# Performance work log

Measured on AMD Instinct MI355X. Metric: run time of the kernel, lower is better.

## Reference

```python
import jax, jax.numpy as jnp
import numpy as np
from jax import lax

B, N, W, F = 16, 2000, 32, 5
TH, SH, HEADS = 128, 64, 4
C = SH // HEADS          # per-head out channels = 16
E_BASE = 32000           # base edges per graph


def setup_inputs():
    key = jax.random.key(0)
    ks = jax.random.split(key, 24)
    rn = lambda k, s, sc=0.05: (jax.random.normal(k, s, jnp.float32) * sc)
    inp = {
        'x': jax.random.normal(ks[0], (B, N, W, F), jnp.float32),
        'base_edge_index': jax.random.randint(ks[1], (2, E_BASE), 0, N, jnp.int64),
        # GRU layer 0 (input F -> TH), layer 1 (TH -> TH); PyTorch gate order r,z,n
        'W_ih0': rn(ks[2], (3 * TH, F)), 'W_hh0': rn(ks[3], (3 * TH, TH)),
        'b_ih0': rn(ks[4], (3 * TH,)),   'b_hh0': rn(ks[5], (3 * TH,)),
        'W_ih1': rn(ks[6], (3 * TH, TH)), 'W_hh1': rn(ks[7], (3 * TH, TH)),
        'b_ih1': rn(ks[8], (3 * TH,)),   'b_hh1': rn(ks[9], (3 * TH,)),
        'ln1_g': jnp.ones((TH,), jnp.float32), 'ln1_b': jnp.zeros((TH,), jnp.float32),
        # GATConv: lin (no bias), att_src/att_dst [H,C], output bias [H*C]
        'gat_W': rn(ks[10], (TH, HEADS * C)),
        'att_src': rn(ks[11], (HEADS, C)), 'att_dst': rn(ks[12], (HEADS, C)),
        'gat_b': rn(ks[13], (HEADS * C,)),
        'ln2_g': jnp.ones((SH,), jnp.float32), 'ln2_b': jnp.zeros((SH,), jnp.float32),
        'reg_W1': rn(ks[14], (SH, 32)), 'reg_b1': rn(ks[15], (32,)),
        'reg_W2': rn(ks[16], (32, 1)),  'reg_b2': rn(ks[17], (1,)),
    }
    return inp


def _gru_layer(xs, W_ih, W_hh, b_ih, b_hh):
    # xs: [W, M, Din] time-major; returns (h_T [M,TH], ys [W,M,TH])
    M = xs.shape[1]
    h0 = jnp.zeros((M, W_hh.shape[1]), xs.dtype)

    def step(h, x_t):
        gi = x_t @ W_ih.T + b_ih
        gh = h @ W_hh.T + b_hh
        i_r, i_z, i_n = jnp.split(gi, 3, axis=-1)
        h_r, h_z, h_n = jnp.split(gh, 3, axis=-1)
        r = jax.nn.sigmoid(i_r + h_r)
        z = jax.nn.sigmoid(i_z + h_z)
        n = jnp.tanh(i_n + r * h_n)
        h_new = (1.0 - z) * n + z * h
        return h_new, h_new

    return lax.scan(step, h0, xs)


def _layernorm(x, g, b, eps=1e-5):
    mu = jnp.mean(x, -1, keepdims=True)
    var = jnp.var(x, -1, keepdims=True)
    return (x - mu) * lax.rsqrt(var + eps) * g + b


def _forward(x, base_edge_index, W_ih0, W_hh0, b_ih0, b_hh0, W_ih1, W_hh1,
             b_ih1, b_hh1, ln1_g, ln1_b, gat_W, att_src, att_dst, gat_b,
             ln2_g, ln2_b, reg_W1, reg_b1, reg_W2, reg_b2):
    Bv, Nv, Wv, Fv = x.shape
    M = Bv * Nv
    xs = x.reshape(M, Wv, Fv).transpose(1, 0, 2)  # [W, M, F] time-major
    _, ys0 = _gru_layer(xs, W_ih0, W_hh0, b_ih0, b_hh0)
    h1, _ = _gru_layer(ys0, W_ih1, W_hh1, b_ih1, b_hh1)  # hidden[-1]: [M, TH]
    temb = _layernorm(h1, ln1_g, ln1_b)

    # batched edge index with per-graph node offsets + self loops (PyG default)
    offs = (jnp.arange(Bv, dtype=base_edge_index.dtype) * Nv)
    eb = (base_edge_index[:, None, :] + offs[None, :, None]).reshape(2, -1)
    loops = jnp.arange(M, dtype=base_edge_index.dtype)
    src = jnp.concatenate([eb[0], loops])
    dst = jnp.concatenate([eb[1], loops])

    # GATConv
    xp = (temb @ gat_W).reshape(M, HEADS, C)                 # [M,H,C]
    a_src = jnp.sum(xp * att_src, -1)                        # [M,H]
    a_dst = jnp.sum(xp * att_dst, -1)
    alpha = jax.nn.leaky_relu(a_src[src] + a_dst[dst], 0.2)  # [E,H]
    amax = jax.ops.segment_max(alpha, dst, num_segments=M)
    ex = jnp.exp(alpha - amax[dst])
    den = jax.ops.segment_sum(ex, dst, num_segments=M)
    w = ex / den[dst]                                        # segment softmax
    agg = jax.ops.segment_sum(w[:, :, None] * xp[src], dst, num_segments=M)
    semb = agg.reshape(M, HEADS * C) + gat_b

    semb = jax.nn.leaky_relu(_layernorm(semb, ln2_g, ln2_b), 0.2)
    h = jax.nn.leaky_relu(semb @ reg_W1 + reg_b1, 0.2)
    pred = h @ reg_W2 + reg_b2                               # [M,1]
    return pred.reshape(Bv, Nv)


def reference(x, base_edge_index, W_ih0, W_hh0, b_ih0, b_hh0, W_ih1, W_hh1,
              b_ih1, b_hh1, ln1_g, ln1_b, gat_W, att_src, att_dst, gat_b,
              ln2_g, ln2_b, reg_W1, reg_b1, reg_W2, reg_b2):
    return _forward(x, base_edge_index, W_ih0, W_hh0, b_ih0, b_hh0, W_ih1,
                    W_hh1, b_ih1, b_hh1, ln1_g, ln1_b, gat_W, att_src,
                    att_dst, gat_b, ln2_g, ln2_b, reg_W1, reg_b1, reg_W2,
                    reg_b2)
```

## Files before the change

kernel.cpp:

```cpp
#include <hip/hip_runtime.h>
#include <math.h>

#define B_   16
#define N_   2000
#define W_   32
#define F_   5
#define TH_  128
#define M_   (B_*N_)
#define SH_  64
#define NPB  128

typedef unsigned short u16;
typedef short short8 __attribute__((ext_vector_type(8)));
typedef float f32x4  __attribute__((ext_vector_type(4)));

__device__ __forceinline__ float leaky_(float x) { return x > 0.0f ? x : 0.2f * x; }
__device__ __forceinline__ float sigm_(float x) {
  return __fdividef(1.0f, 1.0f + __expf(-x));
}
__device__ __forceinline__ float tanh_(float x) {
  const float e2 = __expf(2.0f * x);
  return 1.0f - __fdividef(2.0f, e2 + 1.0f);
}

__device__ __forceinline__ u16 f2bf(float f) {
  unsigned u = __float_as_uint(f);
  unsigned r = (u + 0x7FFFu + ((u >> 16) & 1u)) >> 16;
  return (u16)r;
}
__device__ __forceinline__ u16 f2bf_tr(float f) {
  return (u16)(__float_as_uint(f) >> 16);
}
__device__ __forceinline__ float bf2f(u16 h) { return __uint_as_float(((unsigned)h) << 16); }

__device__ __forceinline__ f32x4 mfma3(short8 ah, short8 al, short8 bh, short8 bl, f32x4 c) {
  c = __builtin_amdgcn_mfma_f32_16x16x32_bf16(ah, bh, c, 0, 0, 0);
  c = __builtin_amdgcn_mfma_f32_16x16x32_bf16(al, bh, c, 0, 0, 0);
  c = __builtin_amdgcn_mfma_f32_16x16x32_bf16(ah, bl, c, 0, 0, 0);
  return c;
}

#define S0_ (384*32)
#define S1_ (384*128)
#define XS_ (M_*W_*8)

__global__ void splitA_kernel(const float* __restrict__ Wih0,
                              u16* __restrict__ wih0h, u16* __restrict__ wih0l)
{
  const int i = blockIdx.x * 256 + threadIdx.x;
  if (i >= S0_) return;
  const int row = i >> 5, k = i & 31;
  const float v = (k < F_) ? Wih0[row * F_ + k] : 0.0f;
  const int g = row >> 7, unit = row & 127, wv = unit >> 4, li = unit & 15;
  const int qq = k >> 3, j = k & 7;
  const int p = ((wv * 3 + g) * 64 + qq * 16 + li) * 8 + j;
  const u16 h = f2bf(v);
  wih0h[p] = h;
  wih0l[p] = f2bf(v - bf2f(h));
}

__global__ __launch_bounds__(256)
void splitB_kernel(const float* __restrict__ Whh0, const float* __restrict__ Wih1,
                   const float* __restrict__ Whh1,
                   u16* __restrict__ wpk, u16* __restrict__ wlo)
{
  const int w = blockIdx.x * 4 + (threadIdx.x >> 6);
  const int lane = threadIdx.x & 63;
  const int mat = w / 384;
  const int r = w - mat * 384;
  const float* src = (mat == 0) ? Whh0 : (mat == 1) ? Wih1 : Whh1;
  const int g = r >> 7, unit = r & 127, wv = unit >> 4, li = unit & 15;

#pragma unroll
  for (int e = 0; e < 2; ++e) {
    const int k = lane * 2 + e;
    const float v = src[r * TH_ + k];
    const u16 h = f2bf(v);
    const u16 l = f2bf(v - bf2f(h));
    const int kt = k >> 5, rem = k & 31, qq = rem >> 3, j = rem & 7;
    const int p = (((wv * 3 + mat) * 4 + kt) * 3 + g) * 512 + (qq * 16 + li) * 8 + j;
    wpk[p] = h;
    wlo[p] = l;
  }
}

__global__ __launch_bounds__(256)
void splitX_kernel(const float* __restrict__ x,
                   u16* __restrict__ xh, u16* __restrict__ xl)
{
  const int tid = blockIdx.x * 256 + threadIdx.x;
  if (tid >= M_ * W_) return;
  const int li = tid & 15, nt = (tid >> 4) & 7, t = (tid >> 7) & 31, mb = tid >> 12;
  const int m = mb * 128 + nt * 16 + li;
  const float* px = x + (size_t)m * (W_ * F_) + t * F_;
  short8 vh, vl;
#pragma unroll
  for (int j = 0; j < 8; ++j) {
    const float v = (j < F_) ? px[j] : 0.0f;
    const u16 h = f2bf_tr(v);
    vh[j] = (short)h;
    vl[j] = (short)f2bf(v - bf2f(h));
  }
  *(short8*)(xh + (size_t)tid * 8) = vh;
  *(short8*)(xl + (size_t)tid * 8) = vl;
}

__global__ __launch_bounds__(512, 2)
void gru_mfma_kernel(const u16* __restrict__ xpkh, const u16* __restrict__ xpkl,
                     const u16* __restrict__ wih0h, const u16* __restrict__ wih0l,
                     const u16* __restrict__ wpk, const u16* __restrict__ wlo,
                     const float* __restrict__ bih0, const float* __restrict__ bhh0,
                     const float* __restrict__ bih1, const float* __restrict__ bhh1,
                     const float* __restrict__ ln1g, const float* __restrict__ ln1b,
                     float* __restrict__ temb)
{
  __shared__ u16 h0hi[NPB * TH_], h0lo[NPB * TH_];
  __shared__ u16 h1hi[NPB * TH_], h1lo[NPB * TH_];

  const int tid = threadIdx.x;
  const int lane = tid & 63, wv = tid >> 6, q = lane >> 4, li = lane & 15;
  const int mbase = blockIdx.x * NPB;
  const int unit = wv * 16 + li;
  const int laneo = lane * 8;
  const int wbase = wv * 18432;

  for (int i = tid; i < NPB * TH_ / 2; i += 512) {
    ((unsigned*)h0hi)[i] = 0u; ((unsigned*)h0lo)[i] = 0u;
    ((unsigned*)h1hi)[i] = 0u; ((unsigned*)h1lo)[i] = 0u;
  }

  const float BR0  = bih0[unit] + bhh0[unit];
  const float BZ0  = bih0[TH_ + unit] + bhh0[TH_ + unit];
  const float BNI0 = bih0[2 * TH_ + unit];
  const float BNH0 = bhh0[2 * TH_ + unit];
  const float BR1  = bih1[unit] + bhh1[unit];
  const float BZ1  = bih1[TH_ + unit] + bhh1[TH_ + unit];
  const float BNI1 = bih1[2 * TH_ + unit];
  const float BNH1 = bhh1[2 * TH_ + unit];
  const f32x4 z4 = {0.0f, 0.0f, 0.0f, 0.0f};
  const short8 z8 = {0, 0, 0, 0, 0, 0, 0, 0};

  short8 bih0h_[3], bih0l_[3];
#pragma unroll
  for (int g = 0; g < 3; ++g) {
    const int ro = (wv * 3 + g) * 512 + laneo;
    bih0h_[g] = *(const short8*)(wih0h + ro);
    bih0l_[g] = *(const short8*)(wih0l + ro);
  }

  int nbase[4];
#pragma unroll
  for (int r = 0; r < 4; ++r)
    nbase[r] = (q * 4 + r) * TH_ + ((((unit >> 3) ^ (q * 4 + r))) << 3) + (unit & 7);

  __syncthreads();

  f32x4 aR[8], aZ[8], aNI[8], aNH[8];

  for (int t = 0; t < W_; ++t) {
    {
      const u16* xbh = xpkh + ((size_t)(blockIdx.x * W_ + t) * 8) * 128 + li * 8;
      const u16* xbl = xpkl + ((size_t)(blockIdx.x * W_ + t) * 8) * 128 + li * 8;
#pragma unroll
      for (int nt = 0; nt < 8; ++nt) {
        short8 xh8 = z8, xl8 = z8;
        if (q == 0) {
          xh8 = *(const short8*)(xbh + nt * 128);
          xl8 = *(const short8*)(xbl + nt * 128);
        }
#pragma unroll
        for (int g = 0; g < 3; ++g) {
          const f32x4 c = mfma3(xh8, xl8, bih0h_[g], bih0l_[g], z4);
          if (g == 0) aR[nt] = c; else if (g == 1) aZ[nt] = c; else aNI[nt] = c;
        }
      }
    }

#pragma unroll
    for (int kt = 0; kt < 4; ++kt) {
      const int off = wbase + kt * 1536 + laneo;
      const short8 bh0 = *(const short8*)(wpk + off);
      const short8 bl0 = *(const short8*)(wlo + off);
      const short8 bh1 = *(const short8*)(wpk + off + 512);
      const short8 bl1 = *(const short8*)(wlo + off + 512);
      const short8 bh2 = *(const short8*)(wpk + off + 1024);
      const short8 bl2 = *(const short8*)(wlo + off + 1024);
      const int ko = ((kt * 4 + q) ^ li) * 8;
#pragma unroll
      for (int nt = 0; nt < 8; ++nt) {
        const int ab = (nt * 16 + li) * TH_ + ko;
        const short8 Ah = *(const short8*)(h0hi + ab);
        const short8 Al = *(const short8*)(h0lo + ab);
        aR[nt] = mfma3(Ah, Al, bh0, bl0, aR[nt]);
        aZ[nt] = mfma3(Ah, Al, bh1, bl1, aZ[nt]);
        aNH[nt] = mfma3(Ah, Al, bh2, bl2, (kt == 0) ? z4 : aNH[nt]);
      }
    }
    __syncthreads();

#pragma unroll
    for (int nt = 0; nt < 8; ++nt)
#pragma unroll
      for (int r = 0; r < 4; ++r) {
        const int idx = nt * 2048 + nbase[r];
        const float hold = bf2f(h0hi[idx]) + bf2f(h0lo[idx]);
        const float rr = sigm_(aR[nt][r] + BR0);
        const float zz = sigm_(aZ[nt][r] + BZ0);
        const float nn = tanh_(aNI[nt][r] + BNI0 + rr * (aNH[nt][r] + BNH0));
        const float hv = (1.0f - zz) * nn + zz * hold;
        const u16 hh = f2bf_tr(hv);
        h0hi[idx] = hh;
        h0lo[idx] = f2bf(hv - bf2f(hh));
      }
    __syncthreads();

#pragma unroll
    for (int kt = 0; kt < 4; ++kt) {
      const int off = wbase + 6144 + kt * 1536 + laneo;
      const short8 bh0 = *(const short8*)(wpk + off);
      const short8 bl0 = *(const short8*)(wlo + off);
      const short8 bh1 = *(const short8*)(wpk + off + 512);
      const short8 bl1 = *(const short8*)(wlo + off + 512);
      const short8 bh2 = *(const short8*)(wpk + off + 1024);
      const short8 bl2 = *(const short8*)(wlo + off + 1024);
      const int ko = ((kt * 4 + q) ^ li) * 8;
#pragma unroll
      for (int nt = 0; nt < 8; ++nt) {
        const int ab = (nt * 16 + li) * TH_ + ko;
        const short8 Ah = *(const short8*)(h0hi + ab);
        const short8 Al = *(const short8*)(h0lo + ab);
        aR[nt]  = mfma3(Ah, Al, bh0, bl0, (kt == 0) ? z4 : aR[nt]);
        aZ[nt]  = mfma3(Ah, Al, bh1, bl1, (kt == 0) ? z4 : aZ[nt]);
        aNI[nt] = mfma3(Ah, Al, bh2, bl2, (kt == 0) ? z4 : aNI[nt]);
      }
    }
#pragma unroll
    for (int kt = 0; kt < 4; ++kt) {
      const int off = wbase + 12288 + kt * 1536 + laneo;
      const short8 bh0 = *(const short8*)(wpk + off);
      const short8 bl0 = *(const short8*)(wlo + off);
      const short8 bh1 = *(const short8*)(wpk + off + 512);
      const short8 bl1 = *(const short8*)(wlo + off + 512);
      const short8 bh2 = *(const short8*)(wpk + off + 1024);
      const short8 bl2 = *(const short8*)(wlo + off + 1024);
      const int ko = ((kt * 4 + q) ^ li) * 8;
#pragma unroll
      for (int nt = 0; nt < 8; ++nt) {
        const int ab = (nt * 16 + li) * TH_ + ko;
        const short8 Ah = *(const short8*)(h1hi + ab);
        const short8 Al = *(const short8*)(h1lo + ab);
        aR[nt]  = mfma3(Ah, Al, bh0, bl0, aR[nt]);
        aZ[nt]  = mfma3(Ah, Al, bh1, bl1, aZ[nt]);
        aNH[nt] = mfma3(Ah, Al, bh2, bl2, (kt == 0) ? z4 : aNH[nt]);
      }
    }
    __syncthreads();

#pragma unroll
    for (int nt = 0; nt < 8; ++nt)
#pragma unroll
      for (int r = 0; r < 4; ++r) {
        const int idx = nt * 2048 + nbase[r];
        const float hold = bf2f(h1hi[idx]) + bf2f(h1lo[idx]);
        const float rr = sigm_(aR[nt][r] + BR1);
        const float zz = sigm_(aZ[nt][r] + BZ1);
        const float nn = tanh_(aNI[nt][r] + BNI1 + rr * (aNH[nt][r] + BNH1));
        const float hv = (1.0f - zz) * nn + zz * hold;
        const u16 hh = f2bf_tr(hv);
        h1hi[idx] = hh;
        h1lo[idx] = f2bf(hv - bf2f(hh));
      }
    __syncthreads();
  }

  const int n = tid >> 2, qq = tid & 3;
  float vr[32];
  float s = 0.0f;
#pragma unroll
  for (int g8 = 0; g8 < 4; ++g8) {
    const int k0 = qq * 32 + g8 * 8;
    const int g16 = (((k0 >> 3) ^ (n & 15))) * 8;
    const short8 hv = *(const short8*)(h1hi + n * TH_ + g16);
    const short8 lv = *(const short8*)(h1lo + n * TH_ + g16);
#pragma unroll
    for (int j = 0; j < 8; ++j) {
      const float f = bf2f((u16)hv[j]) + bf2f((u16)lv[j]);
      vr[g8 * 8 + j] = f;
      s += f;
    }
  }
  s += __shfl_xor(s, 1, 64); s += __shfl_xor(s, 2, 64);
  const float mu = s * (1.0f / TH_);
  float s2 = 0.0f;
#pragma unroll
  for (int k = 0; k < 32; ++k) { const float d = vr[k] - mu; s2 += d * d; }
  s2 += __shfl_xor(s2, 1, 64); s2 += __shfl_xor(s2, 2, 64);
  const float inv = rsqrtf(s2 * (1.0f / TH_) + 1e-5f);
  float* to = temb + (size_t)(mbase + n) * TH_ + qq * 32;
#pragma unroll
  for (int k = 0; k < 32; ++k)
    to[k] = (vr[k] - mu) * inv * ln1g[qq * 32 + k] + ln1b[qq * 32 + k];
}

__global__ __launch_bounds__(256)
void gat_xp_kernel(const float* __restrict__ temb, const float* __restrict__ gatW,
                   const float* __restrict__ attS, const float* __restrict__ attD,
                   float* __restrict__ xp, float* __restrict__ asrc, float* __restrict__ adst)
{
  __shared__ float ts[64][TH_ + 4];
  __shared__ float4 ws4[TH_][16];
  __shared__ float sa[64], sd[64];

  const int tid = threadIdx.x;
  const int mbase = blockIdx.x * 64;

  for (int i = tid; i < 64 * TH_; i += 256) {
    const int n = i >> 7, k = i & 127;
    ts[n][k] = temb[(size_t)mbase * TH_ + i];
  }
  for (int i = tid; i < TH_ * 16; i += 256)
    ((float4*)ws4)[i] = ((const float4*)gatW)[i];
  if (tid < 64) { sa[tid] = attS[tid]; sd[tid] = attD[tid]; }
  __syncthreads();

  const int nl = tid >> 2;
  const int q  = tid & 3;
  float4 acc[4];
#pragma unroll
  for (int i = 0; i < 4; ++i) acc[i] = make_float4(0.f, 0.f, 0.f, 0.f);

  for (int k = 0; k < TH_; ++k) {
    const float tv = ts[nl][k];
#pragma unroll
    for (int c0 = 0; c0 < 4; ++c0) {
      const float4 wv = ws4[k][q * 4 + c0];
      acc[c0].x += tv * wv.x; acc[c0].y += tv * wv.y;
      acc[c0].z += tv * wv.z; acc[c0].w += tv * wv.w;
    }
  }

  float as = 0.0f, ad = 0.0f;
#pragma unroll
  for (int c0 = 0; c0 < 4; ++c0) {
    const int base = q * 16 + c0 * 4;
    as += acc[c0].x * sa[base + 0] + acc[c0].y * sa[base + 1] +
          acc[c0].z * sa[base + 2] + acc[c0].w * sa[base + 3];
    ad += acc[c0].x * sd[base + 0] + acc[c0].y * sd[base + 1] +
          acc[c0].z * sd[base + 2] + acc[c0].w * sd[base + 3];
  }

  const int m = mbase + nl;
  asrc[m * 4 + q] = as;
  adst[m * 4 + q] = ad;
  float4* xpo = (float4*)&xp[(size_t)m * 64 + q * 16];
#pragma unroll
  for (int c0 = 0; c0 < 4; ++c0) xpo[c0] = acc[c0];
}

__global__ void hist_kernel(const int* __restrict__ ei, const int EB, int* __restrict__ cnt)
{
  const int e = blockIdx.x * 256 + threadIdx.x;
  if (e < EB) atomicAdd(&cnt[ei[EB + e]], 1);
}

__global__ void scan_kernel(const int* __restrict__ cnt, int* __restrict__ offs,
                            int* __restrict__ cursor)
{
  __shared__ int part[256];
  const int tid = threadIdx.x;
  const int c0 = tid * 8;
  int loc[8];
  int s = 0;
#pragma unroll
  for (int j = 0; j < 8; ++j) {
    const int idx = c0 + j;
    const int v = (idx < N_) ? cnt[idx] : 0;
    loc[j] = s; s += v;
  }
  part[tid] = s;
  __syncthreads();
  for (int o = 1; o < 256; o <<= 1) {
    const int v = (tid >= o) ? part[tid - o] : 0;
    __syncthreads();
    part[tid] += v;
    __syncthreads();
  }
  const int base = (tid > 0) ? part[tid - 1] : 0;
#pragma unroll
  for (int j = 0; j < 8; ++j) {
    const int idx = c0 + j;
    if (idx < N_) { offs[idx] = base + loc[j]; cursor[idx] = base + loc[j]; }
  }
  if (tid == 255) offs[N_] = part[255];
}

__global__ void fill_kernel(const int* __restrict__ ei, const int EB,
                            int* __restrict__ cursor, int* __restrict__ ssrc)
{
  const int e = blockIdx.x * 256 + threadIdx.x;
  if (e < EB) {
    const int d = ei[EB + e];
    const int p = atomicAdd(&cursor[d], 1);
    ssrc[p] = ei[e];
  }
}

__global__ __launch_bounds__(256)
void gather_kernel(const int* __restrict__ offs, const int* __restrict__ ssrc,
                   const float* __restrict__ asrc, const float* __restrict__ adst,
                   const float* __restrict__ xp,
                   const float* __restrict__ gatb,
                   const float* __restrict__ ln2g, const float* __restrict__ ln2b,
                   const float* __restrict__ W1, const float* __restrict__ b1,
                   const float* __restrict__ W2, const float* __restrict__ b2,
                   float* __restrict__ out)
{
  __shared__ float sW1[SH_ * 32];
  __shared__ float sb1[32], sW2[32];
  __shared__ float ssemb[4][SH_ + 1];

  const int tid = threadIdx.x;
  for (int i = tid; i < SH_ * 32; i += 256) sW1[i] = W1[i];
  if (tid < 32) { sb1[tid] = b1[tid]; sW2[tid] = W2[tid]; }
  __syncthreads();

  const int lane = tid & 63, grp = tid >> 6;
  const int m = blockIdx.x * 4 + grp;
  const int b = m / N_;
  const int n = m - b * N_;
  const int h = lane >> 4;

  const float adv = adst[m * 4 + h];
  const int o0 = offs[n], o1 = offs[n + 1];
  float accn = 0.0f, accd = 0.0f;
  for (int j = o0; j < o1; ++j) {
    const int s = ssrc[j] + b * N_;
    const float a = asrc[s * 4 + h];
    const float ex = __expf(leaky_(a + adv));
    accn += ex * xp[(size_t)s * 64 + lane];
    accd += ex;
  }
  {
    const float a = asrc[m * 4 + h];
    const float ex = __expf(leaky_(a + adv));
    accn += ex * xp[(size_t)m * 64 + lane];
    accd += ex;
  }

  const float v = accn / accd + gatb[lane];
  float s1 = v;
#pragma unroll
  for (int o = 32; o >= 1; o >>= 1) s1 += __shfl_xor(s1, o, 64);
  const float mu = s1 * (1.0f / 64.0f);
  const float d0 = v - mu;
  float s2 = d0 * d0;
#pragma unroll
  for (int o = 32; o >= 1; o >>= 1) s2 += __shfl_xor(s2, o, 64);
  const float var = s2 * (1.0f / 64.0f);
  float sem = d0 * rsqrtf(var + 1e-5f) * ln2g[lane] + ln2b[lane];
  sem = leaky_(sem);

  ssemb[grp][lane] = sem;
  __syncthreads();

  float contrib = 0.0f;
  if (lane < 32) {
    float acc = sb1[lane];
    for (int c = 0; c < SH_; ++c) acc += ssemb[grp][c] * sW1[c * 32 + lane];
    acc = leaky_(acc);
    contrib = acc * sW2[lane];
  }
#pragma unroll
  for (int o = 32; o >= 1; o >>= 1) contrib += __shfl_xor(contrib, o, 64);
  if (lane == 0) out[m] = contrib + b2[0];
}

extern "C" void kernel_launch(void* const* d_in, const int* in_sizes, int n_in,
                              void* d_out, int out_size, void* d_ws, size_t ws_size,
                              hipStream_t stream)
{
  const float* x    = (const float*)d_in[0];
  const int*   ei   = (const int*)d_in[1];
  const float* Wih0 = (const float*)d_in[2];
  const float* Whh0 = (const float*)d_in[3];
  const float* bih0 = (const float*)d_in[4];
  const float* bhh0 = (const float*)d_in[5];
  const float* Wih1 = (const float*)d_in[6];
  const float* Whh1 = (const float*)d_in[7];
  const float* bih1 = (const float*)d_in[8];
  const float* bhh1 = (const float*)d_in[9];
  const float* ln1g = (const float*)d_in[10];
  const float* ln1b = (const float*)d_in[11];
  const float* gatW = (const float*)d_in[12];
  const float* attS = (const float*)d_in[13];
  const float* attD = (const float*)d_in[14];
  const float* gatb = (const float*)d_in[15];
  const float* ln2g = (const float*)d_in[16];
  const float* ln2b = (const float*)d_in[17];
  const float* W1   = (const float*)d_in[18];
  const float* b1   = (const float*)d_in[19];
  const float* W2   = (const float*)d_in[20];
  const float* b2   = (const float*)d_in[21];
  float* out = (float*)d_out;

  const int EB = in_sizes[1] / 2;

  float* ws = (float*)d_ws;
  float* temb = ws;
  float* xp   = temb + (size_t)M_ * TH_;
  float* asrc = xp + (size_t)M_ * 64;
  float* adst = asrc + (size_t)M_ * 4;
  u16*   wh   = (u16*)(adst + (size_t)M_ * 4);
  u16* wih0h = wh;
  u16* wih0l = wh + S0_;
  u16* wpk   = wh + 2 * S0_;
  u16* wlo   = wpk + 3 * S1_;
  u16* xpkh  = wlo + 3 * S1_;
  u16* xpkl  = xpkh + XS_;
  int* cnt    = (int*)(xpkl + XS_);
  int* offs   = cnt + N_;
  int* cursor = offs + N_ + 1;
  int* ssrc   = cursor + N_;

  splitA_kernel<<<(S0_ + 255) / 256, 256, 0, stream>>>(Wih0, wih0h, wih0l);
  splitB_kernel<<<(3 * 384) / 4, 256, 0, stream>>>(Whh0, Wih1, Whh1, wpk, wlo);
  splitX_kernel<<<(M_ * W_) / 256, 256, 0, stream>>>(x, xpkh, xpkl);

  hipMemsetAsync(cnt, 0, N_ * sizeof(int), stream);
  hist_kernel<<<(EB + 255) / 256, 256, 0, stream>>>(ei, EB, cnt);
  scan_kernel<<<1, 256, 0, stream>>>(cnt, offs, cursor);
  fill_kernel<<<(EB + 255) / 256, 256, 0, stream>>>(ei, EB, cursor, ssrc);

  gru_mfma_kernel<<<M_ / NPB, 512, 0, stream>>>(
      xpkh, xpkl, wih0h, wih0l, wpk, wlo,
      bih0, bhh0, bih1, bhh1, ln1g, ln1b, temb);

  gat_xp_kernel<<<M_ / 64, 256, 0, stream>>>(temb, gatW, attS, attD, xp, asrc, adst);

  gather_kernel<<<M_ / 4, 256, 0, stream>>>(offs, ssrc, asrc, adst, xp,
                                            gatb, ln2g, ln2b, W1, b1, W2, b2, out);
}
```

Baseline: 1.483 ms.

## Quantize low-bf16 weight residuals to int8 and software-pipeline weight loads in GRU

The low part of each split-bf16 recurrent weight is now stored as int8 with a per-row scale and decoded in registers, which halves the global/L2 traffic for the residual weights. Weight fragments are double-buffered so the next k-tile's loads are issued before the current tile's MFMAs run. The full __syncthreads barriers are replaced with an LDS-only waitcnt plus s_barrier. The residual loses some precision, and the decode adds ALU work and register pressure.

```diff
diff --git a/kernel.cpp b/kernel.cpp
--- a/kernel.cpp
+++ b/kernel.cpp
@@ -38,6 +38,24 @@
   c = __builtin_amdgcn_mfma_f32_16x16x32_bf16(al, bh, c, 0, 0, 0);
   c = __builtin_amdgcn_mfma_f32_16x16x32_bf16(ah, bl, c, 0, 0, 0);
   return c;
+}
+
+__device__ __forceinline__ short8 dec8(int2 p, float s) {
+  short8 r;
+#pragma unroll
+  for (int j = 0; j < 4; ++j) {
+    const int e0 = (int)(signed char)((p.x >> (8 * j)) & 0xFF);
+    const int e1 = (int)(signed char)((p.y >> (8 * j)) & 0xFF);
+    r[j]     = (short)(__float_as_uint((float)e0 * s) >> 16);
+    r[4 + j] = (short)(__float_as_uint((float)e1 * s) >> 16);
+  }
+  return r;
+}
+
+__device__ __forceinline__ void bar_lds() {
+  asm volatile("s_waitcnt lgkmcnt(0)" ::: "memory");
+  __builtin_amdgcn_s_barrier();
+  asm volatile("" ::: "memory");
 }
 
 #define S0_ (384*32)
@@ -62,7 +80,8 @@
 __global__ __launch_bounds__(256)
 void splitB_kernel(const float* __restrict__ Whh0, const float* __restrict__ Wih1,
                    const float* __restrict__ Whh1,
-                   u16* __restrict__ wpk, u16* __restrict__ wlo)
+                   u16* __restrict__ wpk, signed char* __restrict__ wq,
+                   float* __restrict__ sInv)
 {
   const int w = blockIdx.x * 4 + (threadIdx.x >> 6);
   const int lane = threadIdx.x & 63;
@@ -71,17 +90,29 @@
   const float* src = (mat == 0) ? Whh0 : (mat == 1) ? Wih1 : Whh1;
   const int g = r >> 7, unit = r & 127, wv = unit >> 4, li = unit & 15;
 
-#pragma unroll
-  for (int e = 0; e < 2; ++e) {
-    const int k = lane * 2 + e;
-    const float v = src[r * TH_ + k];
-    const u16 h = f2bf(v);
-    const u16 l = f2bf(v - bf2f(h));
-    const int kt = k >> 5, rem = k & 31, qq = rem >> 3, j = rem & 7;
+  const float v0 = src[r * TH_ + lane * 2];
+  const float v1 = src[r * TH_ + lane * 2 + 1];
+  const u16 h0 = f2bf(v0), h1 = f2bf(v1);
+  const float l0 = v0 - bf2f(h0), l1 = v1 - bf2f(h1);
+  float m = fmaxf(fabsf(l0), fabsf(l1));
+#pragma unroll
+  for (int o = 32; o >= 1; o >>= 1) m = fmaxf(m, __shfl_xor(m, o, 64));
+  const float s = (m > 0.0f) ? __fdividef(127.0f, m) : 0.0f;
+  int q0 = (int)rintf(l0 * s), q1 = (int)rintf(l1 * s);
+  q0 = max(-127, min(127, q0)); q1 = max(-127, min(127, q1));
+
+  const int k0 = lane * 2, k1 = lane * 2 + 1;
+  {
+    const int kt = k0 >> 5, rem = k0 & 31, qq = rem >> 3, j = rem & 7;
     const int p = (((wv * 3 + mat) * 4 + kt) * 3 + g) * 512 + (qq * 16 + li) * 8 + j;
-    wpk[p] = h;
-    wlo[p] = l;
-  }
+    wpk[p] = h0; wq[p] = (signed char)q0;
+  }
+  {
+    const int kt = k1 >> 5, rem = k1 & 31, qq = rem >> 3, j = rem & 7;
+    const int p = (((wv * 3 + mat) * 4 + kt) * 3 + g) * 512 + (qq * 16 + li) * 8 + j;
+    wpk[p] = h1; wq[p] = (signed char)q1;
+  }
+  if (lane == 0) sInv[mat * 384 + r] = (m > 0.0f) ? m * (1.0f / 127.0f) : 0.0f;
 }
 
 __global__ __launch_bounds__(256)
@@ -91,7 +122,7 @@
   const int tid = blockIdx.x * 256 + threadIdx.x;
   if (tid >= M_ * W_) return;
   const int li = tid & 15, nt = (tid >> 4) & 7, t = (tid >> 7) & 31, mb = tid >> 12;
-  const int m = mb * 128 + nt * 16 + li;
+  const int m = mb * NPB + nt * 16 + li;
   const float* px = x + (size_t)m * (W_ * F_) + t * F_;
   short8 vh, vl;
 #pragma unroll
@@ -105,10 +136,20 @@
   *(short8*)(xl + (size_t)tid * 8) = vl;
 }
 
+#define WPREF(PN)                                                       \
+  { const int o_ = wbase + (PN) * 1536 + laneo;                         \
+    wbh[(PN) & 1][0] = *(const short8*)(wpk + o_);                      \
+    wbh[(PN) & 1][1] = *(const short8*)(wpk + o_ + 512);                \
+    wbh[(PN) & 1][2] = *(const short8*)(wpk + o_ + 1024);               \
+    wbq[(PN) & 1][0] = *(const int2*)(wqk + o_);                        \
+    wbq[(PN) & 1][1] = *(const int2*)(wqk + o_ + 512);                  \
+    wbq[(PN) & 1][2] = *(const int2*)(wqk + o_ + 1024); }
+
 __global__ __launch_bounds__(512, 2)
 void gru_mfma_kernel(const u16* __restrict__ xpkh, const u16* __restrict__ xpkl,
                      const u16* __restrict__ wih0h, const u16* __restrict__ wih0l,
-                     const u16* __restrict__ wpk, const u16* __restrict__ wlo,
+                     const u16* __restrict__ wpk, const signed char* __restrict__ wqk,
+                     const float* __restrict__ sInv,
                      const float* __restrict__ bih0, const float* __restrict__ bhh0,
                      const float* __restrict__ bih1, const float* __restrict__ bhh1,
                      const float* __restrict__ ln1g, const float* __restrict__ ln1b,
@@ -129,6 +170,13 @@
     ((unsigned*)h1hi)[i] = 0u; ((unsigned*)h1lo)[i] = 0u;
   }
 
+  float si0[3], si1[3], si2[3];
+#pragma unroll
+  for (int g = 0; g < 3; ++g) {
+    si0[g] = sInv[0 * 384 + g * TH_ + unit];
+    si1[g] = sInv[1 * 384 + g * TH_ + unit];
+    si2[g] = sInv[2 * 384 + g * TH_ + unit];
+  }
   const float BR0  = bih0[unit] + bhh0[unit];
   const float BZ0  = bih0[TH_ + unit] + bhh0[TH_ + unit];
   const float BNI0 = bih0[2 * TH_ + unit];
@@ -153,7 +201,11 @@
   for (int r = 0; r < 4; ++r)
     nbase[r] = (q * 4 + r) * TH_ + ((((unit >> 3) ^ (q * 4 + r))) << 3) + (unit & 7);
 
-  __syncthreads();
+  short8 wbh[2][3];
+  int2   wbq[2][3];
+  WPREF(0);
+
+  bar_lds();
 
   f32x4 aR[8], aZ[8], aNI[8], aNH[8];
 
@@ -178,25 +230,23 @@
 
 #pragma unroll
     for (int kt = 0; kt < 4; ++kt) {
-      const int off = wbase + kt * 1536 + laneo;
-      const short8 bh0 = *(const short8*)(wpk + off);
-      const short8 bl0 = *(const short8*)(wlo + off);
-      const short8 bh1 = *(const short8*)(wpk + off + 512);
-      const short8 bl1 = *(const short8*)(wlo + off + 512);
-      const short8 bh2 = *(const short8*)(wpk + off + 1024);
-      const short8 bl2 = *(const short8*)(wlo + off + 1024);
+      WPREF(kt + 1);
+      const short8 bh0 = wbh[kt & 1][0], bh1 = wbh[kt & 1][1], bh2 = wbh[kt & 1][2];
+      const short8 bl0 = dec8(wbq[kt & 1][0], si0[0]);
+      const short8 bl1 = dec8(wbq[kt & 1][1], si0[1]);
+      const short8 bl2 = dec8(wbq[kt & 1][2], si0[2]);
       const int ko = ((kt * 4 + q) ^ li) * 8;
 #pragma unroll
       for (int nt = 0; nt < 8; ++nt) {
         const int ab = (nt * 16 + li) * TH_ + ko;
         const short8 Ah = *(const short8*)(h0hi + ab);
         const short8 Al = *(const short8*)(h0lo + ab);
-        aR[nt] = mfma3(Ah, Al, bh0, bl0, aR[nt]);
-        aZ[nt] = mfma3(Ah, Al, bh1, bl1, aZ[nt]);
+        aR[nt]  = mfma3(Ah, Al, bh0, bl0, aR[nt]);
+        aZ[nt]  = mfma3(Ah, Al, bh1, bl1, aZ[nt]);
         aNH[nt] = mfma3(Ah, Al, bh2, bl2, (kt == 0) ? z4 : aNH[nt]);
       }
     }
-    __syncthreads();
+    bar_lds();
 
 #pragma unroll
     for (int nt = 0; nt < 8; ++nt)
@@ -212,17 +262,16 @@
         h0hi[idx] = hh;
         h0lo[idx] = f2bf(hv - bf2f(hh));
       }
-    __syncthreads();
+    bar_lds();
 
 #pragma unroll
     for (int kt = 0; kt < 4; ++kt) {
-      const int off = wbase + 6144 + kt * 1536 + laneo;
-      const short8 bh0 = *(const short8*)(wpk + off);
-      const short8 bl0 = *(const short8*)(wlo + off);
-      const short8 bh1 = *(const short8*)(wpk + off + 512);
-      const short8 bl1 = *(const short8*)(wlo + off + 512);
-      const short8 bh2 = *(const short8*)(wpk + off + 1024);
-      const short8 bl2 = *(const short8*)(wlo + off + 1024);
+      const int p = 4 + kt;
+      WPREF(p + 1);
+      const short8 bh0 = wbh[p & 1][0], bh1 = wbh[p & 1][1], bh2 = wbh[p & 1][2];
+      const short8 bl0 = dec8(wbq[p & 1][0], si1[0]);
+      const short8 bl1 = dec8(wbq[p & 1][1], si1[1]);
+      const short8 bl2 = dec8(wbq[p & 1][2], si1[2]);
       const int ko = ((kt * 4 + q) ^ li) * 8;
 #pragma unroll
       for (int nt = 0; nt < 8; ++nt) {
@@ -236,13 +285,12 @@
     }
 #pragma unroll
     for (int kt = 0; kt < 4; ++kt) {
-      const int off = wbase + 12288 + kt * 1536 + laneo;
-      const short8 bh0 = *(const short8*)(wpk + off);
-      const short8 bl0 = *(const short8*)(wlo + off);
-      const short8 bh1 = *(const short8*)(wpk + off + 512);
-      const short8 bl1 = *(const short8*)(wlo + off + 512);
-      const short8 bh2 = *(const short8*)(wpk + off + 1024);
-      const short8 bl2 = *(const short8*)(wlo + off + 1024);
+      const int p = 8 + kt;
+      WPREF((p + 1) % 12);
+      const short8 bh0 = wbh[p & 1][0], bh1 = wbh[p & 1][1], bh2 = wbh[p & 1][2];
+      const short8 bl0 = dec8(wbq[p & 1][0], si2[0]);
+      const short8 bl1 = dec8(wbq[p & 1][1], si2[1]);
+      const short8 bl2 = dec8(wbq[p & 1][2], si2[2]);
       const int ko = ((kt * 4 + q) ^ li) * 8;
 #pragma unroll
       for (int nt = 0; nt < 8; ++nt) {
@@ -254,7 +302,7 @@
         aNH[nt] = mfma3(Ah, Al, bh2, bl2, (kt == 0) ? z4 : aNH[nt]);
       }
     }
-    __syncthreads();
+    bar_lds();
 
 #pragma unroll
     for (int nt = 0; nt < 8; ++nt)
@@ -270,7 +318,7 @@
         h1hi[idx] = hh;
         h1lo[idx] = f2bf(hv - bf2f(hh));
       }
-    __syncthreads();
+    bar_lds();
   }
 
   const int n = tid >> 2, qq = tid & 3;
@@ -514,8 +562,9 @@
   u16* wih0h = wh;
   u16* wih0l = wh + S0_;
   u16* wpk   = wh + 2 * S0_;
-  u16* wlo   = wpk + 3 * S1_;
-  u16* xpkh  = wlo + 3 * S1_;
+  float* sInv = (float*)(wpk + 3 * S1_);
+  signed char* wq = (signed char*)(sInv + 3 * 384);
+  u16* xpkh  = (u16*)(wq + 3 * S1_);
   u16* xpkl  = xpkh + XS_;
   int* cnt    = (int*)(xpkl + XS_);
   int* offs   = cnt + N_;
@@ -523,7 +572,7 @@
   int* ssrc   = cursor + N_;
 
   splitA_kernel<<<(S0_ + 255) / 256, 256, 0, stream>>>(Wih0, wih0h, wih0l);
-  splitB_kernel<<<(3 * 384) / 4, 256, 0, stream>>>(Whh0, Wih1, Whh1, wpk, wlo);
+  splitB_kernel<<<(3 * 384) / 4, 256, 0, stream>>>(Whh0, Wih1, Whh1, wpk, wq, sInv);
   splitX_kernel<<<(M_ * W_) / 256, 256, 0, stream>>>(x, xpkh, xpkl);
 
   hipMemsetAsync(cnt, 0, N_ * sizeof(int), stream);
@@ -532,7 +581,7 @@
   fill_kernel<<<(EB + 255) / 256, 256, 0, stream>>>(ei, EB, cursor, ssrc);
 
   gru_mfma_kernel<<<M_ / NPB, 512, 0, stream>>>(
-      xpkh, xpkl, wih0h, wih0l, wpk, wlo,
+      xpkh, xpkl, wih0h, wih0l, wpk, wq, sInv,
       bih0, bhh0, bih1, bhh1, ln1g, ln1b, temb);
 
   gat_xp_kernel<<<M_ / 64, 256, 0, stream>>>(temb, gatW, attS, attD, xp, asrc, adst);
```

New measurement: 1.618 ms. 9.0% more time.

## Double-buffer GRU weight fragments in registers and use LDS-only barriers

Applied to the files above, without the earlier changes.

Each 128x128 GRU weight tile, as hi/lo bf16 fragments, is now loaded one k-phase ahead into a two-slot register buffer across all 12 matmul phases of a timestep, so global load latency hides behind MFMA work. The layer-1 phases are reordered (recurrent h1 part first) so the prefetch chain wraps cleanly into the next timestep. __syncthreads is replaced by a barrier that waits only on LDS counters, so in-flight weight prefetches are not drained at each barrier. The redundant barrier at the end of each timestep is dropped. The extra live registers for the buffers risk spills or lower occupancy under the 512x2 launch bounds.

```diff
diff --git a/kernel.cpp b/kernel.cpp
--- a/kernel.cpp
+++ b/kernel.cpp
@@ -38,6 +38,12 @@
   c = __builtin_amdgcn_mfma_f32_16x16x32_bf16(al, bh, c, 0, 0, 0);
   c = __builtin_amdgcn_mfma_f32_16x16x32_bf16(ah, bl, c, 0, 0, 0);
   return c;
+}
+
+__device__ __forceinline__ void bar_lds() {
+  asm volatile("s_waitcnt lgkmcnt(0)" ::: "memory");
+  __builtin_amdgcn_s_barrier();
+  asm volatile("" ::: "memory");
 }
 
 #define S0_ (384*32)
@@ -91,7 +97,7 @@
   const int tid = blockIdx.x * 256 + threadIdx.x;
   if (tid >= M_ * W_) return;
   const int li = tid & 15, nt = (tid >> 4) & 7, t = (tid >> 7) & 31, mb = tid >> 12;
-  const int m = mb * 128 + nt * 16 + li;
+  const int m = mb * NPB + nt * 16 + li;
   const float* px = x + (size_t)m * (W_ * F_) + t * F_;
   short8 vh, vl;
 #pragma unroll
@@ -104,6 +110,18 @@
   *(short8*)(xh + (size_t)tid * 8) = vh;
   *(short8*)(xl + (size_t)tid * 8) = vl;
 }
+
+#define POFF(P) ((P) < 4 ? (P) * 1536 : ((P) < 8 ? 12288 + ((P) - 4) * 1536 \
+                                                 : 6144 + ((P) - 8) * 1536))
+
+#define WPREF(PN)                                                       \
+  { const int o_ = wbase + POFF(PN) + laneo;                            \
+    wbh[(PN) & 1][0] = *(const short8*)(wpk + o_);                      \
+    wbh[(PN) & 1][1] = *(const short8*)(wpk + o_ + 512);                \
+    wbh[(PN) & 1][2] = *(const short8*)(wpk + o_ + 1024);               \
+    wbl[(PN) & 1][0] = *(const short8*)(wlo + o_);                      \
+    wbl[(PN) & 1][1] = *(const short8*)(wlo + o_ + 512);                \
+    wbl[(PN) & 1][2] = *(const short8*)(wlo + o_ + 1024); }
 
 __global__ __launch_bounds__(512, 2)
 void gru_mfma_kernel(const u16* __restrict__ xpkh, const u16* __restrict__ xpkl,
@@ -153,7 +171,11 @@
   for (int r = 0; r < 4; ++r)
     nbase[r] = (q * 4 + r) * TH_ + ((((unit >> 3) ^ (q * 4 + r))) << 3) + (unit & 7);
 
-  __syncthreads();
+  short8 wbh[2][3];
+  short8 wbl[2][3];
+  WPREF(0);
+
+  bar_lds();
 
   f32x4 aR[8], aZ[8], aNI[8], aNH[8];
 
@@ -178,25 +200,21 @@
 
 #pragma unroll
     for (int kt = 0; kt < 4; ++kt) {
-      const int off = wbase + kt * 1536 + laneo;
-      const short8 bh0 = *(const short8*)(wpk + off);
-      const short8 bl0 = *(const short8*)(wlo + off);
-      const short8 bh1 = *(const short8*)(wpk + off + 512);
-      const short8 bl1 = *(const short8*)(wlo + off + 512);
-      const short8 bh2 = *(const short8*)(wpk + off + 1024);
-      const short8 bl2 = *(const short8*)(wlo + off + 1024);
+      WPREF(kt + 1);
+      const short8 bh0 = wbh[kt & 1][0], bh1 = wbh[kt & 1][1], bh2 = wbh[kt & 1][2];
+      const short8 bl0 = wbl[kt & 1][0], bl1 = wbl[kt & 1][1], bl2 = wbl[kt & 1][2];
       const int ko = ((kt * 4 + q) ^ li) * 8;
 #pragma unroll
       for (int nt = 0; nt < 8; ++nt) {
         const int ab = (nt * 16 + li) * TH_ + ko;
         const short8 Ah = *(const short8*)(h0hi + ab);
         const short8 Al = *(const short8*)(h0lo + ab);
-        aR[nt] = mfma3(Ah, Al, bh0, bl0, aR[nt]);
-        aZ[nt] = mfma3(Ah, Al, bh1, bl1, aZ[nt]);
+        aR[nt]  = mfma3(Ah, Al, bh0, bl0, aR[nt]);
+        aZ[nt]  = mfma3(Ah, Al, bh1, bl1, aZ[nt]);
         aNH[nt] = mfma3(Ah, Al, bh2, bl2, (kt == 0) ? z4 : aNH[nt]);
       }
     }
-    __syncthreads();
+    bar_lds();
 
 #pragma unroll
     for (int nt = 0; nt < 8; ++nt)
@@ -212,49 +230,43 @@
         h0hi[idx] = hh;
         h0lo[idx] = f2bf(hv - bf2f(hh));
       }
-    __syncthreads();
+    bar_lds();
 
 #pragma unroll
     for (int kt = 0; kt < 4; ++kt) {
-      const int off = wbase + 6144 + kt * 1536 + laneo;
-      const short8 bh0 = *(const short8*)(wpk + off);
-      const short8 bl0 = *(const short8*)(wlo + off);
-      const short8 bh1 = *(const short8*)(wpk + off + 512);
-      const short8 bl1 = *(const short8*)(wlo + off + 512);
-      const short8 bh2 = *(const short8*)(wpk + off + 1024);
-      const short8 bl2 = *(const short8*)(wlo + off + 1024);
+      const int p = 4 + kt;
+      WPREF(p + 1);
+      const short8 bh0 = wbh[p & 1][0], bh1 = wbh[p & 1][1], bh2 = wbh[p & 1][2];
+      const short8 bl0 = wbl[p & 1][0], bl1 = wbl[p & 1][1], bl2 = wbl[p & 1][2];
+      const int ko = ((kt * 4 + q) ^ li) * 8;
+#pragma unroll
+      for (int nt = 0; nt < 8; ++nt) {
+        const int ab = (nt * 16 + li) * TH_ + ko;
+        const short8 Ah = *(const short8*)(h1hi + ab);
+        const short8 Al = *(const short8*)(h1lo + ab);
+        aR[nt]  = mfma3(Ah, Al, bh0, bl0, (kt == 0) ? z4 : aR[nt]);
+        aZ[nt]  = mfma3(Ah, Al, bh1, bl1, (kt == 0) ? z4 : aZ[nt]);
+        aNH[nt] = mfma3(Ah, Al, bh2, bl2, (kt == 0) ? z4 : aNH[nt]);
+      }
+    }
+#pragma unroll
+    for (int kt = 0; kt < 4; ++kt) {
+      const int p = 8 + kt;
+      WPREF((p + 1) % 12);
+      const short8 bh0 = wbh[p & 1][0], bh1 = wbh[p & 1][1], bh2 = wbh[p & 1][2];
+      const short8 bl0 = wbl[p & 1][0], bl1 = wbl[p & 1][1], bl2 = wbl[p & 1][2];
       const int ko = ((kt * 4 + q) ^ li) * 8;
 #pragma unroll
       for (int nt = 0; nt < 8; ++nt) {
         const int ab = (nt * 16 + li) * TH_ + ko;
         const short8 Ah = *(const short8*)(h0hi + ab);
         const short8 Al = *(const short8*)(h0lo + ab);
-        aR[nt]  = mfma3(Ah, Al, bh0, bl0, (kt == 0) ? z4 : aR[nt]);
-        aZ[nt]  = mfma3(Ah, Al, bh1, bl1, (kt == 0) ? z4 : aZ[nt]);
+        aR[nt]  = mfma3(Ah, Al, bh0, bl0, aR[nt]);
+        aZ[nt]  = mfma3(Ah, Al, bh1, bl1, aZ[nt]);
         aNI[nt] = mfma3(Ah, Al, bh2, bl2, (kt == 0) ? z4 : aNI[nt]);
       }
     }
-#pragma unroll
-    for (int kt = 0; kt < 4; ++kt) {
-      const int off = wbase + 12288 + kt * 1536 + laneo;
-      const short8 bh0 = *(const short8*)(wpk + off);
-      const short8 bl0 = *(const short8*)(wlo + off);
-      const short8 bh1 = *(const short8*)(wpk + off + 512);
-      const short8 bl1 = *(const short8*)(wlo + off + 512);
-      const short8 bh2 = *(const short8*)(wpk + off + 1024);
-      const short8 bl2 = *(const short8*)(wlo + off + 1024);
-      const int ko = ((kt * 4 + q) ^ li) * 8;
-#pragma unroll
-      for (int nt = 0; nt < 8; ++nt) {
-        const int ab = (nt * 16 + li) * TH_ + ko;
-        const short8 Ah = *(const short8*)(h1hi + ab);
-        const short8 Al = *(const short8*)(h1lo + ab);
-        aR[nt]  = mfma3(Ah, Al, bh0, bl0, aR[nt]);
-        aZ[nt]  = mfma3(Ah, Al, bh1, bl1, aZ[nt]);
-        aNH[nt] = mfma3(Ah, Al, bh2, bl2, (kt == 0) ? z4 : aNH[nt]);
-      }
-    }
-    __syncthreads();
+    bar_lds();
 
 #pragma unroll
     for (int nt = 0; nt < 8; ++nt)
@@ -270,8 +282,8 @@
         h1hi[idx] = hh;
         h1lo[idx] = f2bf(hv - bf2f(hh));
       }
-    __syncthreads();
-  }
+  }
+  bar_lds();
 
   const int n = tid >> 2, qq = tid & 3;
   float vr[32];
```

Measured after the change: 1.441 ms. 1.03x faster.
